# Kernel optimization log

Measured on AMD Instinct MI355X. Metric: run time of the kernel, lower is better.

Reference implementation:

```python
import jax, jax.numpy as jnp
import numpy as np

B, N = 256, 131072

def setup_inputs() -> dict:
    key = jax.random.key(0)
    kx, km = jax.random.split(key)
    x = jax.random.normal(kx, (B, N), dtype=jnp.float32)
    mask = jax.random.randint(km, (B, N), 0, 2).astype(jnp.bool_)
    return {"x": x, "mask": mask}

def reference(x, mask):
    # Masked cumulative sum along dim=1: zero out masked-off entries, then scan.
    return jnp.cumsum(jnp.where(mask, x, 0.0), axis=1)
```

## Files before the change

### kernel.cpp

```cpp
#include <hip/hip_runtime.h>


#define N_ROWS   256
#define N_COLS   131072
#define BLOCK    1024
#define VEC      4
#define TILE     (BLOCK * VEC)
#define NTILES   (N_COLS / TILE)
#define NWAVES   (BLOCK / 64)

__global__ __launch_bounds__(BLOCK)
void masked_cumsum_kernel(const float* __restrict__ x,
                          const int* __restrict__ mask,
                          float* __restrict__ out) {
    __shared__ float waveSums[2][NWAVES];

    const int row  = blockIdx.x;
    const int tid  = threadIdx.x;
    const int lane = tid & 63;
    const int wave = tid >> 6;

    const size_t rowBase = (size_t)row * N_COLS;
    const float4* __restrict__ x4 = (const float4*)(x + rowBase);
    const int4*   __restrict__ m4 = (const int4*)(mask + rowBase);
    float4*       __restrict__ o4 = (float4*)(out + rowBase);

    float carry = 0.0f;

    float4 xv = x4[tid];
    int4   mv = m4[tid];

    for (int t = 0; t < NTILES; ++t) {
        const float4 cx = xv;
        const int4   cm = mv;

        if (t + 1 < NTILES) {
            const int nidx = (t + 1) * BLOCK + tid;
            xv = x4[nidx];
            mv = m4[nidx];
        }

        const float v0 = cm.x ? cx.x : 0.0f;
        const float v1 = cm.y ? cx.y : 0.0f;
        const float v2 = cm.z ? cx.z : 0.0f;
        const float v3 = cm.w ? cx.w : 0.0f;
        const float s0 = v0;
        const float s1 = s0 + v1;
        const float s2 = s1 + v2;
        const float s3 = s2 + v3;
        const float tsum = s3;

        float incl = tsum;
        #pragma unroll
        for (int d = 1; d < 64; d <<= 1) {
            const float y = __shfl_up(incl, d, 64);
            if (lane >= d) incl += y;
        }
        const float waveExcl = incl - tsum;

        if (lane == 63) waveSums[t & 1][wave] = incl;
        __syncthreads();

        float waveOff = 0.0f, tileTot = 0.0f;
        #pragma unroll
        for (int w = 0; w < NWAVES; ++w) {
            const float s = waveSums[t & 1][w];
            if (w < wave) waveOff += s;
            tileTot += s;
        }

        const float base = carry + waveOff + waveExcl;
        float4 r;
        r.x = base + s0;
        r.y = base + s1;
        r.z = base + s2;
        r.w = base + s3;
        o4[t * BLOCK + tid] = r;

        carry += tileTot;
    }
}

extern "C" void kernel_launch(void* const* d_in, const int* in_sizes, int n_in,
                              void* d_out, int out_size, void* d_ws, size_t ws_size,
                              hipStream_t stream) {
    const float* x    = (const float*)d_in[0];
    const int*   mask = (const int*)d_in[1];
    float*       out  = (float*)d_out;
    (void)in_sizes; (void)n_in; (void)out_size; (void)d_ws; (void)ws_size;

    masked_cumsum_kernel<<<N_ROWS, BLOCK, 0, stream>>>(x, mask, out);
}
```

Before: 316.5 us.

## Process four chunks per wave per barrier with nontemporal stores

Each wave now handles four consecutive 256-element chunks per super-tile, scanning them serially inside the wave with a wave-level carry. This cuts block-wide barriers and shared-memory reductions by four and keeps more loads in flight per thread. Output is written with nontemporal stores and the barrier is a raw s_barrier after an lgkmcnt wait. The cost is higher register pressure, and the launch-bounds hint may force spilling.

```diff
diff --git a/kernel.cpp b/kernel.cpp
--- a/kernel.cpp
+++ b/kernel.cpp
@@ -1,83 +1,132 @@
 #include <hip/hip_runtime.h>
+#include <stdint.h>
 
 
-#define N_ROWS   256
-#define N_COLS   131072
-#define BLOCK    1024
-#define VEC      4
-#define TILE     (BLOCK * VEC)
-#define NTILES   (N_COLS / TILE)
-#define NWAVES   (BLOCK / 64)
+#define B_ROWS  256
+#define N_COLS  131072
+#define BLOCK   1024
+#define NWAVES  16
+#define CHUNKS  4
+#define STILE   (NWAVES * 64 * 4 * CHUNKS)
+#define NST     (N_COLS / STILE)
 
-__global__ __launch_bounds__(BLOCK)
-void masked_cumsum_kernel(const float* __restrict__ x,
-                          const int* __restrict__ mask,
-                          float* __restrict__ out) {
-    __shared__ float waveSums[2][NWAVES];
+typedef float nativef4 __attribute__((ext_vector_type(4)));
 
-    const int row  = blockIdx.x;
+__device__ __forceinline__ float wave_incl_scan(float v, int lane) {
+    #pragma unroll
+    for (int d = 1; d < 64; d <<= 1) {
+        const float y = __shfl_up(v, d, 64);
+        if (lane >= d) v += y;
+    }
+    return v;
+}
+
+__global__ __launch_bounds__(BLOCK, 4)
+void masked_cumsum_fused(const float* __restrict__ x,
+                         const int*   __restrict__ mask,
+                         float*       __restrict__ out)
+{
+    __shared__ float wsum[2][NWAVES];
+
     const int tid  = threadIdx.x;
     const int lane = tid & 63;
     const int wave = tid >> 6;
+    const int row  = blockIdx.x;
 
     const size_t rowBase = (size_t)row * N_COLS;
     const float4* __restrict__ x4 = (const float4*)(x + rowBase);
     const int4*   __restrict__ m4 = (const int4*)(mask + rowBase);
-    float4*       __restrict__ o4 = (float4*)(out + rowBase);
+    nativef4*     __restrict__ o4 = (nativef4*)(out + rowBase);
 
-    float carry = 0.0f;
+    const int tb = wave * 256 + lane;
 
-    float4 xv = x4[tid];
-    int4   mv = m4[tid];
+    float4 x0 = x4[tb];          int4 m0 = m4[tb];
+    float4 x1 = x4[tb + 64];     int4 m1 = m4[tb + 64];
+    float4 x2 = x4[tb + 128];    int4 m2 = m4[tb + 128];
+    float4 x3 = x4[tb + 192];    int4 m3 = m4[tb + 192];
 
-    for (int t = 0; t < NTILES; ++t) {
-        const float4 cx = xv;
-        const int4   cm = mv;
+    float rowCarry = 0.0f;
 
-        if (t + 1 < NTILES) {
-            const int nidx = (t + 1) * BLOCK + tid;
-            xv = x4[nidx];
-            mv = m4[nidx];
+    for (int st = 0; st < NST; ++st) {
+        const int nb = (st + 1) * 4096 + tb;
+        const bool more = (st + 1 < NST);
+        float wcarry = 0.0f;
+        nativef4 rv0, rv1, rv2, rv3;
+
+        {
+            const float v0 = m0.x ? x0.x : 0.0f;
+            const float v1 = m0.y ? x0.y : 0.0f;
+            const float v2 = m0.z ? x0.z : 0.0f;
+            const float v3 = m0.w ? x0.w : 0.0f;
+            if (more) { x0 = x4[nb]; m0 = m4[nb]; }
+            const float s0 = v0, s1 = s0 + v1, s2 = s1 + v2, s3 = s2 + v3;
+            const float incl = wave_incl_scan(s3, lane);
+            const float base = wcarry + (incl - s3);
+            rv0.x = base + s0; rv0.y = base + s1; rv0.z = base + s2; rv0.w = base + s3;
+            wcarry += __shfl(incl, 63, 64);
+        }
+        {
+            const float v0 = m1.x ? x1.x : 0.0f;
+            const float v1 = m1.y ? x1.y : 0.0f;
+            const float v2 = m1.z ? x1.z : 0.0f;
+            const float v3 = m1.w ? x1.w : 0.0f;
+            if (more) { x1 = x4[nb + 64]; m1 = m4[nb + 64]; }
+            const float s0 = v0, s1 = s0 + v1, s2 = s1 + v2, s3 = s2 + v3;
+            const float incl = wave_incl_scan(s3, lane);
+            const float base = wcarry + (incl - s3);
+            rv1.x = base + s0; rv1.y = base + s1; rv1.z = base + s2; rv1.w = base + s3;
+            wcarry += __shfl(incl, 63, 64);
+        }
+        {
+            const float v0 = m2.x ? x2.x : 0.0f;
+            const float v1 = m2.y ? x2.y : 0.0f;
+            const float v2 = m2.z ? x2.z : 0.0f;
+            const float v3 = m2.w ? x2.w : 0.0f;
+            if (more) { x2 = x4[nb + 128]; m2 = m4[nb + 128]; }
+            const float s0 = v0, s1 = s0 + v1, s2 = s1 + v2, s3 = s2 + v3;
+            const float incl = wave_incl_scan(s3, lane);
+            const float base = wcarry + (incl - s3);
+            rv2.x = base + s0; rv2.y = base + s1; rv2.z = base + s2; rv2.w = base + s3;
+            wcarry += __shfl(incl, 63, 64);
+        }
+        {
+            const float v0 = m3.x ? x3.x : 0.0f;
+            const float v1 = m3.y ? x3.y : 0.0f;
+            const float v2 = m3.z ? x3.z : 0.0f;
+            const float v3 = m3.w ? x3.w : 0.0f;
+            if (more) { x3 = x4[nb + 192]; m3 = m4[nb + 192]; }
+            const float s0 = v0, s1 = s0 + v1, s2 = s1 + v2, s3 = s2 + v3;
+            const float incl = wave_incl_scan(s3, lane);
+            const float base = wcarry + (incl - s3);
+            rv3.x = base + s0; rv3.y = base + s1; rv3.z = base + s2; rv3.w = base + s3;
+            wcarry += __shfl(incl, 63, 64);
         }
 
-        const float v0 = cm.x ? cx.x : 0.0f;
-        const float v1 = cm.y ? cx.y : 0.0f;
-        const float v2 = cm.z ? cx.z : 0.0f;
-        const float v3 = cm.w ? cx.w : 0.0f;
-        const float s0 = v0;
-        const float s1 = s0 + v1;
-        const float s2 = s1 + v2;
-        const float s3 = s2 + v3;
-        const float tsum = s3;
+        if (lane == 0) wsum[st & 1][wave] = wcarry;
+        asm volatile("s_waitcnt lgkmcnt(0)" ::: "memory");
+        __builtin_amdgcn_s_barrier();
+        asm volatile("" ::: "memory");
 
-        float incl = tsum;
-        #pragma unroll
-        for (int d = 1; d < 64; d <<= 1) {
-            const float y = __shfl_up(incl, d, 64);
-            if (lane >= d) incl += y;
-        }
-        const float waveExcl = incl - tsum;
-
-        if (lane == 63) waveSums[t & 1][wave] = incl;
-        __syncthreads();
-
-        float waveOff = 0.0f, tileTot = 0.0f;
+        float woff = 0.0f, btot = 0.0f;
         #pragma unroll
         for (int w = 0; w < NWAVES; ++w) {
-            const float s = waveSums[t & 1][w];
-            if (w < wave) waveOff += s;
-            tileTot += s;
+            const float s = wsum[st & 1][w];
+            if (w < wave) woff += s;
+            btot += s;
         }
+        const float addv = rowCarry + woff;
 
-        const float base = carry + waveOff + waveExcl;
-        float4 r;
-        r.x = base + s0;
-        r.y = base + s1;
-        r.z = base + s2;
-        r.w = base + s3;
-        o4[t * BLOCK + tid] = r;
+        const int ob = st * 4096 + tb;
+        rv0.x += addv; rv0.y += addv; rv0.z += addv; rv0.w += addv;
+        rv1.x += addv; rv1.y += addv; rv1.z += addv; rv1.w += addv;
+        rv2.x += addv; rv2.y += addv; rv2.z += addv; rv2.w += addv;
+        rv3.x += addv; rv3.y += addv; rv3.z += addv; rv3.w += addv;
+        __builtin_nontemporal_store(rv0, &o4[ob]);
+        __builtin_nontemporal_store(rv1, &o4[ob + 64]);
+        __builtin_nontemporal_store(rv2, &o4[ob + 128]);
+        __builtin_nontemporal_store(rv3, &o4[ob + 192]);
 
-        carry += tileTot;
+        rowCarry += btot;
     }
 }
 
@@ -89,5 +138,5 @@
     float*       out  = (float*)d_out;
     (void)in_sizes; (void)n_in; (void)out_size; (void)d_ws; (void)ws_size;
 
-    masked_cumsum_kernel<<<N_ROWS, BLOCK, 0, stream>>>(x, mask, out);
+    masked_cumsum_fused<<<B_ROWS, BLOCK, 0, stream>>>(x, mask, out);
 }
```

Result: slower. 323.0 us (+2.1%).

## Deepen register prefetch to four tiles and use raw barrier without vmcnt wait

Applied to the files above, without the earlier changes.

Keeps four tiles of x and mask in flight in registers instead of one, so more global loads are outstanding per row block while earlier tiles are scanned. It also swaps __syncthreads for an explicit lgkmcnt wait plus s_barrier, so the barrier does not also wait for pending vector-memory loads and prefetches can keep running across it. The cost is higher register pressure and a larger unrolled body. Only 256 blocks run, one per row, so per-block memory-level parallelism is the bottleneck this targets.

```diff
diff --git a/kernel.cpp b/kernel.cpp
--- a/kernel.cpp
+++ b/kernel.cpp
@@ -1,4 +1,5 @@
 #include <hip/hip_runtime.h>
+#include <stdint.h>
 
 
 #define N_ROWS   256
@@ -8,17 +9,19 @@
 #define TILE     (BLOCK * VEC)
 #define NTILES   (N_COLS / TILE)
 #define NWAVES   (BLOCK / 64)
+#define DEPTH    4
 
-__global__ __launch_bounds__(BLOCK)
-void masked_cumsum_kernel(const float* __restrict__ x,
-                          const int* __restrict__ mask,
-                          float* __restrict__ out) {
-    __shared__ float waveSums[2][NWAVES];
+__global__ __launch_bounds__(BLOCK, 4)
+void masked_cumsum_deep(const float* __restrict__ x,
+                        const int*   __restrict__ mask,
+                        float*       __restrict__ out)
+{
+    __shared__ float wsum[2][NWAVES];
 
-    const int row  = blockIdx.x;
     const int tid  = threadIdx.x;
     const int lane = tid & 63;
     const int wave = tid >> 6;
+    const int row  = blockIdx.x;
 
     const size_t rowBase = (size_t)row * N_COLS;
     const float4* __restrict__ x4 = (const float4*)(x + rowBase);
@@ -27,58 +30,64 @@
 
     float carry = 0.0f;
 
-    float4 xv = x4[tid];
-    int4   mv = m4[tid];
+    float4 xa = x4[tid];              int4 ma = m4[tid];
+    float4 xb = x4[BLOCK + tid];      int4 mb = m4[BLOCK + tid];
+    float4 xc = x4[2 * BLOCK + tid];  int4 mc = m4[2 * BLOCK + tid];
+    float4 xd = x4[3 * BLOCK + tid];  int4 md = m4[3 * BLOCK + tid];
 
-    for (int t = 0; t < NTILES; ++t) {
-        const float4 cx = xv;
-        const int4   cm = mv;
+    #define STEP(XS, MS, T)                                                  \
+    do {                                                                     \
+        const float4 cx = XS;                                                \
+        const int4   cm = MS;                                                \
+        if ((T) + DEPTH < NTILES) {                                          \
+            const int ni = ((T) + DEPTH) * BLOCK + tid;                      \
+            XS = x4[ni];                                                     \
+            MS = m4[ni];                                                     \
+        }                                                                    \
+        const float v0 = cm.x ? cx.x : 0.0f;                                 \
+        const float v1 = cm.y ? cx.y : 0.0f;                                 \
+        const float v2 = cm.z ? cx.z : 0.0f;                                 \
+        const float v3 = cm.w ? cx.w : 0.0f;                                 \
+        const float s0 = v0;                                                 \
+        const float s1 = s0 + v1;                                            \
+        const float s2 = s1 + v2;                                            \
+        const float s3 = s2 + v3;                                            \
+        float incl = s3;                                                     \
+        _Pragma("unroll")                                                    \
+        for (int d = 1; d < 64; d <<= 1) {                                   \
+            const float y = __shfl_up(incl, d, 64);                          \
+            if (lane >= d) incl += y;                                        \
+        }                                                                    \
+        const float wexcl = incl - s3;                                       \
+        if (lane == 63) wsum[(T) & 1][wave] = incl;                          \
+        asm volatile("s_waitcnt lgkmcnt(0)" ::: "memory");                   \
+        __builtin_amdgcn_s_barrier();                                        \
+        asm volatile("" ::: "memory");                                       \
+        float woff = 0.0f, ttot = 0.0f;                                      \
+        _Pragma("unroll")                                                    \
+        for (int w = 0; w < NWAVES; ++w) {                                   \
+            const float s = wsum[(T) & 1][w];                                \
+            if (w < wave) woff += s;                                         \
+            ttot += s;                                                       \
+        }                                                                    \
+        const float basev = carry + woff + wexcl;                            \
+        float4 r;                                                            \
+        r.x = basev + s0;                                                    \
+        r.y = basev + s1;                                                    \
+        r.z = basev + s2;                                                    \
+        r.w = basev + s3;                                                    \
+        o4[(T) * BLOCK + tid] = r;                                           \
+        carry += ttot;                                                       \
+    } while (0)
 
-        if (t + 1 < NTILES) {
-            const int nidx = (t + 1) * BLOCK + tid;
-            xv = x4[nidx];
-            mv = m4[nidx];
-        }
-
-        const float v0 = cm.x ? cx.x : 0.0f;
-        const float v1 = cm.y ? cx.y : 0.0f;
-        const float v2 = cm.z ? cx.z : 0.0f;
-        const float v3 = cm.w ? cx.w : 0.0f;
-        const float s0 = v0;
-        const float s1 = s0 + v1;
-        const float s2 = s1 + v2;
-        const float s3 = s2 + v3;
-        const float tsum = s3;
-
-        float incl = tsum;
-        #pragma unroll
-        for (int d = 1; d < 64; d <<= 1) {
-            const float y = __shfl_up(incl, d, 64);
-            if (lane >= d) incl += y;
-        }
-        const float waveExcl = incl - tsum;
-
-        if (lane == 63) waveSums[t & 1][wave] = incl;
-        __syncthreads();
-
-        float waveOff = 0.0f, tileTot = 0.0f;
-        #pragma unroll
-        for (int w = 0; w < NWAVES; ++w) {
-            const float s = waveSums[t & 1][w];
-            if (w < wave) waveOff += s;
-            tileTot += s;
-        }
-
-        const float base = carry + waveOff + waveExcl;
-        float4 r;
-        r.x = base + s0;
-        r.y = base + s1;
-        r.z = base + s2;
-        r.w = base + s3;
-        o4[t * BLOCK + tid] = r;
-
-        carry += tileTot;
+    for (int g = 0; g < NTILES / DEPTH; ++g) {
+        const int t0 = g * DEPTH;
+        STEP(xa, ma, t0 + 0);
+        STEP(xb, mb, t0 + 1);
+        STEP(xc, mc, t0 + 2);
+        STEP(xd, md, t0 + 3);
     }
+    #undef STEP
 }
 
 extern "C" void kernel_launch(void* const* d_in, const int* in_sizes, int n_in,
@@ -89,5 +98,5 @@
     float*       out  = (float*)d_out;
     (void)in_sizes; (void)n_in; (void)out_size; (void)d_ws; (void)ws_size;
 
-    masked_cumsum_kernel<<<N_ROWS, BLOCK, 0, stream>>>(x, mask, out);
+    masked_cumsum_deep<<<N_ROWS, BLOCK, 0, stream>>>(x, mask, out);
 }
```

Measured after the change: 313.9 us. About the same (-0.8%).
